# Optimization experiments

Measured on AMD Instinct MI355X. Metric: run time of the kernel, lower is better.

Reference implementation:

```python
import jax, jax.numpy as jnp
import numpy as np

# module hyperparams (init_kwargs)
OUTLINER_RATIO_1 = 0.01
OUTLINER_RATIO_2 = 0.01
SUB_OUTLINER_RATIO_2 = 0.2
SUB_OUTLINER_BIT_2 = 8
RANK = 16


def setup_inputs() -> dict:
    key = jax.random.key(0)
    k1, k2 = jax.random.split(key)
    B, H, S, D = 2, 16, 2048, 128
    # x1 is a softmax output (attention probabilities): rows sum to 1, values in [0,1]
    logits = jax.random.normal(k1, (B, H, S, S), dtype=jnp.float32)
    x1 = jax.nn.softmax(logits, axis=-1)
    x2 = jax.random.normal(k2, (B, H, S, D), dtype=jnp.float32)
    return {"x1": x1, "x2": x2}


def get_statistics_softmax(x, outliner_ratio):
    # kth-value threshold on first batch element (torch.kthvalue, 1-indexed)
    v = jnp.sort(x[0].reshape(-1))
    k = int(v.size * (1.0 - outliner_ratio))
    return v[k - 1]


def get_statistics_x2(x, outliner_ratio, sub_ratio, bit):
    x0 = x[0]  # [H, S, D]
    D = x0.shape[-1]
    a = jnp.abs(x0).reshape(-1)
    k = int(a.size * (1.0 - outliner_ratio))
    outliner = jnp.sort(a)[k - 1]
    # residual after removing outliers; rank columns by L2 norm
    resid = jnp.where(jnp.abs(x0) > outliner, 0.0, x0).reshape(-1, D)
    col_norm = jnp.linalg.norm(resid, axis=0)  # [D]
    n_cols = max(1, int(sub_ratio * D))
    _, cols = jax.lax.top_k(col_norm, n_cols)  # max-norm column list (static size)
    sub = resid[:, cols]
    qmax = float(2 ** (bit - 1) - 1)
    scale = jnp.max(jnp.abs(sub)) / qmax
    return outliner, cols, scale


def prune_softmax(x, outliner):
    return jnp.where(x > outliner, x, 0.0)


def fake_divide_outliner_suboutlinear_svd(x, outliner, cols, scale, rank, bit):
    # 1) split out outliers (kept exactly)
    x_out = jnp.where(jnp.abs(x) > outliner, x, 0.0)
    r = x - x_out
    # 2) rank-`rank` SVD approximation of the residual (batched over B,H)
    U, Sv, Vt = jnp.linalg.svd(r, full_matrices=False)
    x_lr = (U[..., :rank] * Sv[..., None, :rank]) @ Vt[..., :rank, :]
    r2 = r - x_lr
    # 3) fake-quantize the high-norm (sub-outlier) columns at `bit` bits; drop the rest
    qmax = float(2 ** (bit - 1) - 1)
    sub_q = jnp.clip(jnp.round(r2[..., cols] / scale), -qmax - 1.0, qmax) * scale
    r_q = jnp.zeros_like(r2).at[..., cols].set(sub_q)
    return x_out + x_lr + r_q


def reference(x1, x2):
    # iteration = 0 (< 10): compute statistics branch of EfficientMemoryGEMMWithSoftmaxFunc.forward
    result = x1 @ x2
    outliner_1 = get_statistics_softmax(x1, OUTLINER_RATIO_1)
    outliner_2, cols_2, scale_2 = get_statistics_x2(
        x2, OUTLINER_RATIO_2, SUB_OUTLINER_RATIO_2, SUB_OUTLINER_BIT_2)
    # The pruned/compressed tensors are computed (saved for backward in torch);
    # forward output matches Func.forward's returns.
    _x1p = prune_softmax(x1, outliner_1)
    _x2c = fake_divide_outliner_suboutlinear_svd(
        x2, outliner_2, cols_2, scale_2, RANK, SUB_OUTLINER_BIT_2)
    return (result, outliner_1, outliner_2, cols_2, scale_2)
```

## Files before the change

### kernel.cpp

```cpp
#include <hip/hip_runtime.h>

typedef __bf16 bf16x8 __attribute__((ext_vector_type(8)));
typedef unsigned short u16x8 __attribute__((ext_vector_type(8)));
typedef float f32x4 __attribute__((ext_vector_type(4)));

#define S_DIM 2048
#define D_DIM 128
#define N1 67108864LL
#define N2 4194304LL
#define RANK1 66437774u
#define RANK2 4152359u

#define OUT_O1 8388608
#define OUT_O2 8388609
#define OUT_COLS 8388610
#define OUT_SCALE 8388635

#define WS_H0 0
#define WS_H1 2048
#define WS_H2 4096
#define WS_H3 6144
#define WS_STATE 6656
#define WS_SUMSQ 6672
#define WS_CMAX 6800
#define WS_TICKET 6928
#define WS_TOTAL 8192

__device__ __forceinline__ unsigned long long pack4c(float x, float y, float z, float w) {
  union { unsigned long long u; __bf16 h[4]; } cv;
  cv.h[0] = (__bf16)x; cv.h[1] = (__bf16)y; cv.h[2] = (__bf16)z; cv.h[3] = (__bf16)w;
  return cv.u;
}

__global__ void init_ws(unsigned* __restrict__ ws) {
  int i = blockIdx.x * 256 + threadIdx.x;
  if (i < WS_TOTAL) ws[i] = (i == WS_STATE) ? RANK2 : 0u;
}

#define LDA 40

__global__ __launch_bounds__(256, 2) void gemm_kernel(
    const float* __restrict__ x1, const float* __restrict__ x2,
    float* __restrict__ out, unsigned* __restrict__ ws) {
  __shared__ __align__(16) unsigned short lA[128 * LDA];
  __shared__ __align__(16) unsigned short lB[128 * LDA];
  __shared__ unsigned lh[4][2048];
  __shared__ unsigned lh2[2048];
  __shared__ unsigned ps[256];
  __shared__ unsigned lastt;

  const int bid = blockIdx.x;
  const int bh = (bid & 7) + ((bid >> 7) << 3);
  const int mt = (bid >> 3) & 15;
  const int t = threadIdx.x;
  const int lane = t & 63;
  const int wave = t >> 6;
  const int wm = (wave >> 1) * 64;
  const int wn = (wave & 1) * 64;
  const int l15 = lane & 15;
  const int quad = lane >> 4;
  const bool do_hist = (bh < 16);

  unsigned* myh = lh[wave];
  if (do_hist) {
    for (int i = lane; i < 2048; i += 64) myh[i] = 0u;
    for (int i = t; i < 2048; i += 256) lh2[i] = 0u;
  }
  __syncthreads();

  const float* Ag = x1 + (long long)bh * S_DIM * S_DIM + (long long)mt * 128 * S_DIM;
  const float* Bg = x2 + (long long)bh * S_DIM * D_DIM;
  float* Cg = out + (long long)bh * S_DIM * D_DIM + (long long)mt * 128 * D_DIM;

  f32x4 acc[4][4];
#pragma unroll
  for (int i = 0; i < 4; ++i)
#pragma unroll
    for (int j = 0; j < 4; ++j) acc[i][j] = f32x4{0.f, 0.f, 0.f, 0.f};

  const int a_seg = t & 7;
  const int a_row = t >> 3;
  const int bcol = t & 127;
  const int b_kq = t >> 7;

  float4 a_c[4], b_c[4];
#pragma unroll
  for (int p = 0; p < 4; ++p)
    a_c[p] = *reinterpret_cast<const float4*>(Ag + (long long)(a_row + p * 32) * S_DIM + a_seg * 4);
#pragma unroll
  for (int g = 0; g < 4; ++g) {
    int k0 = b_kq * 16 + g * 4;
    long long base = (long long)k0 * D_DIM + bcol;
    b_c[g].x = Bg[base];
    b_c[g].y = Bg[base + D_DIM];
    b_c[g].z = Bg[base + 2 * D_DIM];
    b_c[g].w = Bg[base + 3 * D_DIM];
  }

  for (int kb = 0; kb < S_DIM; kb += 32) {
    float4 a_p[4], b_p[4];
    const bool pf = (kb + 32 < S_DIM);
    if (pf) {
#pragma unroll
      for (int p = 0; p < 4; ++p)
        a_p[p] = *reinterpret_cast<const float4*>(
            Ag + (long long)(a_row + p * 32) * S_DIM + (kb + 32) + a_seg * 4);
#pragma unroll
      for (int g = 0; g < 4; ++g) {
        int k0 = b_kq * 16 + g * 4;
        long long base = (long long)(kb + 32 + k0) * D_DIM + bcol;
        b_p[g].x = Bg[base];
        b_p[g].y = Bg[base + D_DIM];
        b_p[g].z = Bg[base + 2 * D_DIM];
        b_p[g].w = Bg[base + 3 * D_DIM];
      }
    }

#pragma unroll
    for (int p = 0; p < 4; ++p) {
      int row = a_row + p * 32;
      *reinterpret_cast<unsigned long long*>(&lA[row * LDA + a_seg * 4]) =
          pack4c(a_c[p].x, a_c[p].y, a_c[p].z, a_c[p].w);
    }
#pragma unroll
    for (int g = 0; g < 4; ++g) {
      int k0 = b_kq * 16 + g * 4;
      *reinterpret_cast<unsigned long long*>(&lB[bcol * LDA + k0]) =
          pack4c(b_c[g].x, b_c[g].y, b_c[g].z, b_c[g].w);
    }

    if (do_hist) {
#pragma unroll
      for (int p = 0; p < 4; ++p) {
        atomicAdd(&myh[__float_as_uint(a_c[p].x) >> 19], 1u);
        atomicAdd(&myh[__float_as_uint(a_c[p].y) >> 19], 1u);
        atomicAdd(&myh[__float_as_uint(a_c[p].z) >> 19], 1u);
        atomicAdd(&myh[__float_as_uint(a_c[p].w) >> 19], 1u);
      }
      if ((kb >> 7) == mt) {
#pragma unroll
        for (int g = 0; g < 4; ++g) {
          atomicAdd(&lh2[(__float_as_uint(b_c[g].x) & 0x7FFFFFFFu) >> 20], 1u);
          atomicAdd(&lh2[(__float_as_uint(b_c[g].y) & 0x7FFFFFFFu) >> 20], 1u);
          atomicAdd(&lh2[(__float_as_uint(b_c[g].z) & 0x7FFFFFFFu) >> 20], 1u);
          atomicAdd(&lh2[(__float_as_uint(b_c[g].w) & 0x7FFFFFFFu) >> 20], 1u);
        }
      }
    }
    __syncthreads();

    bf16x8 af[4], bfr[4];
#pragma unroll
    for (int i = 0; i < 4; ++i) {
      af[i] = __builtin_bit_cast(bf16x8,
          *reinterpret_cast<const u16x8*>(&lA[(wm + i * 16 + l15) * LDA + quad * 8]));
      bfr[i] = __builtin_bit_cast(bf16x8,
          *reinterpret_cast<const u16x8*>(&lB[(wn + i * 16 + l15) * LDA + quad * 8]));
    }
#pragma unroll
    for (int i = 0; i < 4; ++i)
#pragma unroll
      for (int j = 0; j < 4; ++j)
        acc[i][j] = __builtin_amdgcn_mfma_f32_16x16x32_bf16(af[i], bfr[j], acc[i][j], 0, 0, 0);
    __syncthreads();

    if (pf) {
#pragma unroll
      for (int p = 0; p < 4; ++p) a_c[p] = a_p[p];
#pragma unroll
      for (int g = 0; g < 4; ++g) b_c[g] = b_p[g];
    }
  }

#pragma unroll
  for (int i = 0; i < 4; ++i) {
#pragma unroll
    for (int j = 0; j < 4; ++j) {
      int row0 = wm + i * 16 + quad * 4;
      int col = wn + j * 16 + l15;
#pragma unroll
      for (int r = 0; r < 4; ++r)
        Cg[(long long)(row0 + r) * D_DIM + col] = acc[i][j][r];
    }
  }

  if (do_hist) {
    for (int i = t; i < 2048; i += 256) {
      unsigned s = lh[0][i] + lh[1][i] + lh[2][i] + lh[3][i];
      if (s) atomicAdd(&ws[WS_H0 + i], s);
      unsigned s2 = lh2[i];
      if (s2) atomicAdd(&ws[WS_H1 + i], s2);
    }
  }
  __threadfence();
  __syncthreads();
  if (t == 0) lastt = atomicAdd(&ws[WS_TICKET + 0], 1u);
  __syncthreads();
  if (lastt != 511u) return;

  {
    unsigned v[8];
    unsigned s = 0;
#pragma unroll
    for (int j = 0; j < 8; ++j) { v[j] = atomicAdd(&ws[WS_H0 + t * 8 + j], 0u); s += v[j]; }
    ps[t] = s;
    __syncthreads();
    for (int off = 1; off < 256; off <<= 1) {
      unsigned add = (t >= off) ? ps[t - off] : 0u;
      __syncthreads();
      ps[t] += add;
      __syncthreads();
    }
    unsigned incl = ps[t];
    unsigned before = incl - s;
    if (RANK1 >= before && RANK1 < incl) {
      unsigned rr = RANK1 - before;
      for (int j = 0; j < 8; ++j) {
        if (rr < v[j]) {
          unsigned b = (unsigned)(t * 8 + j);
          float lo = __uint_as_float(b << 19);
          float hi = __uint_as_float((b + 1u) << 19);
          out[OUT_O1] = lo + (hi - lo) * (((float)rr + 0.5f) / (float)v[j]);
          break;
        }
        rr -= v[j];
      }
    }
  }
  __syncthreads();

  {
    unsigned v[8];
    unsigned s = 0;
#pragma unroll
    for (int j = 0; j < 8; ++j) { v[j] = atomicAdd(&ws[WS_H1 + t * 8 + j], 0u); s += v[j]; }
    ps[t] = s;
    __syncthreads();
    for (int off = 1; off < 256; off <<= 1) {
      unsigned add = (t >= off) ? ps[t - off] : 0u;
      __syncthreads();
      ps[t] += add;
      __syncthreads();
    }
    unsigned incl = ps[t];
    unsigned before = incl - s;
    if (RANK2 >= before && RANK2 < incl) {
      unsigned rr = RANK2 - before;
      for (int j = 0; j < 8; ++j) {
        if (rr < v[j]) {
          ws[WS_STATE + 0] = rr;
          ws[WS_STATE + 1] = (unsigned)(t * 8 + j);
          break;
        }
        rr -= v[j];
      }
    }
  }
}

__global__ void x2_pass(const float* __restrict__ x2, unsigned* __restrict__ ws,
                        float* __restrict__ out, int phase) {
  __shared__ unsigned lh[2048];
  __shared__ unsigned ps[256];
  __shared__ unsigned lastt;
  unsigned* h = ws + ((phase == 2) ? WS_H2 : WS_H3);
  unsigned* state = ws + WS_STATE;
  const int nb = (phase == 3) ? 512 : 2048;
  const int t = threadIdx.x;
  for (int i = t; i < nb; i += 256) lh[i] = 0u;
  __syncthreads();
  const unsigned b1 = state[1];
  const unsigned pfx2 = (state[1] << 11) | state[2];
  long long i0 = (long long)(blockIdx.x * 256 + t) * 4;
  long long stride = (long long)gridDim.x * 1024;
  for (long long i = i0; i < N2; i += stride) {
    float4 v = *reinterpret_cast<const float4*>(x2 + i);
    float fv[4] = {v.x, v.y, v.z, v.w};
#pragma unroll
    for (int j = 0; j < 4; ++j) {
      unsigned key = __float_as_uint(fv[j]) & 0x7FFFFFFFu;
      if (phase == 2) {
        if ((key >> 20) == b1) atomicAdd(&lh[(key >> 9) & 0x7FFu], 1u);
      } else {
        if ((key >> 9) == pfx2) atomicAdd(&lh[key & 0x1FFu], 1u);
      }
    }
  }
  __syncthreads();
  for (int i = t; i < nb; i += 256)
    if (lh[i]) atomicAdd(&h[i], lh[i]);
  __threadfence();
  __syncthreads();
  if (t == 0) lastt = atomicAdd(&ws[WS_TICKET + ((phase == 2) ? 1 : 2)], 1u);
  __syncthreads();
  if (lastt != 255u) return;

  const int per = nb >> 8;
  const unsigned r = state[0];
  const unsigned sb1 = state[1];
  const unsigned sb2 = state[2];
  unsigned v[8];
  unsigned s = 0;
  for (int j = 0; j < per; ++j) { v[j] = atomicAdd(&h[t * per + j], 0u); s += v[j]; }
  ps[t] = s;
  __syncthreads();
  for (int off = 1; off < 256; off <<= 1) {
    unsigned add = (t >= off) ? ps[t - off] : 0u;
    __syncthreads();
    ps[t] += add;
    __syncthreads();
  }
  unsigned incl = ps[t];
  unsigned before = incl - s;
  if (r >= before && r < incl) {
    unsigned rr = r - before;
    for (int j = 0; j < per; ++j) {
      if (rr < v[j]) {
        unsigned b = (unsigned)(t * per + j);
        if (phase == 2) {
          state[0] = rr;
          state[2] = b;
        } else {
          unsigned bits = (sb1 << 20) | (sb2 << 9) | b;
          state[3] = bits;
          out[OUT_O2] = __uint_as_float(bits);
        }
        break;
      }
      rr -= v[j];
    }
  }
}

__global__ void colnorm_kernel(const float* __restrict__ x2, unsigned* __restrict__ ws,
                               float* __restrict__ out) {
  __shared__ float red[256];
  __shared__ unsigned redm[256];
  __shared__ float vv[128];
  __shared__ float rv[128];
  __shared__ int ri[128];
  __shared__ unsigned cmv[128];
  __shared__ unsigned lastt;
  unsigned* state = ws + WS_STATE;
  float* sumsq = (float*)(ws + WS_SUMSQ);
  unsigned* cmax = ws + WS_CMAX;
  const float thr = __uint_as_float(state[3]);
  const int t = threadIdx.x;
  const int c = t & 127;
  const int half = t >> 7;
  float local = 0.f;
  unsigned lmax = 0u;
  for (int i = 0; i < 64; ++i) {
    int row = blockIdx.x * 128 + i * 2 + half;
    float x = x2[(long long)row * 128 + c];
    float a = fabsf(x);
    if (a <= thr) {
      local += x * x;
      unsigned ab = __float_as_uint(a);
      if (ab > lmax) lmax = ab;
    }
  }
  red[t] = local;
  redm[t] = lmax;
  __syncthreads();
  if (half == 0) {
    atomicAdd(&sumsq[c], red[c] + red[c + 128]);
    unsigned m = redm[c] > redm[c + 128] ? redm[c] : redm[c + 128];
    if (m) atomicMax(&cmax[c], m);
  }
  __threadfence();
  __syncthreads();
  if (t == 0) lastt = atomicAdd(&ws[WS_TICKET + 3], 1u);
  __syncthreads();
  if (lastt != 255u) return;

  if (t < 128) {
    vv[t] = atomicAdd(&sumsq[t], 0.0f);
    cmv[t] = atomicMax(&cmax[t], 0u);
  }
  __syncthreads();
  unsigned smax = 0u;
  for (int s2 = 0; s2 < 25; ++s2) {
    if (t < 128) { rv[t] = vv[t]; ri[t] = t; }
    __syncthreads();
    for (int off = 64; off >= 1; off >>= 1) {
      if (t < off) {
        float a = rv[t], b = rv[t + off];
        int ia = ri[t], ib = ri[t + off];
        if (b > a || (b == a && ib < ia)) { rv[t] = b; ri[t] = ib; }
      }
      __syncthreads();
    }
    if (t == 0) {
      int cc = ri[0];
      out[OUT_COLS + s2] = (float)cc;
      vv[cc] = -1.0f;
      if (cmv[cc] > smax) smax = cmv[cc];
    }
    __syncthreads();
  }
  if (t == 0) out[OUT_SCALE] = __uint_as_float(smax) / 127.0f;
}

extern "C" void kernel_launch(void* const* d_in, const int* in_sizes, int n_in,
                              void* d_out, int out_size, void* d_ws, size_t ws_size,
                              hipStream_t stream) {
  (void)in_sizes; (void)n_in; (void)out_size; (void)ws_size;
  const float* x1 = (const float*)d_in[0];
  const float* x2 = (const float*)d_in[1];
  float* out = (float*)d_out;
  unsigned* ws = (unsigned*)d_ws;

  init_ws<<<32, 256, 0, stream>>>(ws);
  gemm_kernel<<<512, 256, 0, stream>>>(x1, x2, out, ws);
  x2_pass<<<256, 256, 0, stream>>>(x2, ws, out, 2);
  x2_pass<<<256, 256, 0, stream>>>(x2, ws, out, 3);
  colnorm_kernel<<<256, 256, 0, stream>>>(x2, ws, out);
}
```

Baseline: 927.0 us.

## Move x2 histogram and threshold finalization out of GEMM into separate pass

Removes the x2 magnitude histogram, the last-block ticket, and the softmax kth-value finalization from the GEMM kernel, and moves them into a new x2_pass1 kernel launched after the GEMM. The GEMM also drops its separate prefetch registers: it issues the next tile's global loads after the LDS stores and histogram atomics, so register pressure and shared memory use fall. The cost is one extra kernel launch and a second read of x2.

```diff
diff --git a/kernel.cpp b/kernel.cpp
--- a/kernel.cpp
+++ b/kernel.cpp
@@ -41,13 +41,10 @@
 
 __global__ __launch_bounds__(256, 2) void gemm_kernel(
     const float* __restrict__ x1, const float* __restrict__ x2,
-    float* __restrict__ out, unsigned* __restrict__ ws) {
+    float* __restrict__ out, unsigned* __restrict__ hist) {
   __shared__ __align__(16) unsigned short lA[128 * LDA];
   __shared__ __align__(16) unsigned short lB[128 * LDA];
   __shared__ unsigned lh[4][2048];
-  __shared__ unsigned lh2[2048];
-  __shared__ unsigned ps[256];
-  __shared__ unsigned lastt;
 
   const int bid = blockIdx.x;
   const int bh = (bid & 7) + ((bid >> 7) << 3);
@@ -64,9 +61,7 @@
   unsigned* myh = lh[wave];
   if (do_hist) {
     for (int i = lane; i < 2048; i += 64) myh[i] = 0u;
-    for (int i = t; i < 2048; i += 256) lh2[i] = 0u;
-  }
-  __syncthreads();
+  }
 
   const float* Ag = x1 + (long long)bh * S_DIM * S_DIM + (long long)mt * 128 * S_DIM;
   const float* Bg = x2 + (long long)bh * S_DIM * D_DIM;
@@ -80,71 +75,61 @@
 
   const int a_seg = t & 7;
   const int a_row = t >> 3;
-  const int bcol = t & 127;
+  const int b_n = t & 127;
   const int b_kq = t >> 7;
 
-  float4 a_c[4], b_c[4];
+  float4 a_r[4];
+  float4 b_r[4];
 #pragma unroll
   for (int p = 0; p < 4; ++p)
-    a_c[p] = *reinterpret_cast<const float4*>(Ag + (long long)(a_row + p * 32) * S_DIM + a_seg * 4);
+    a_r[p] = *reinterpret_cast<const float4*>(Ag + (long long)(a_row + p * 32) * S_DIM + a_seg * 4);
 #pragma unroll
   for (int g = 0; g < 4; ++g) {
     int k0 = b_kq * 16 + g * 4;
-    long long base = (long long)k0 * D_DIM + bcol;
-    b_c[g].x = Bg[base];
-    b_c[g].y = Bg[base + D_DIM];
-    b_c[g].z = Bg[base + 2 * D_DIM];
-    b_c[g].w = Bg[base + 3 * D_DIM];
+    long long base = (long long)k0 * D_DIM + b_n;
+    b_r[g].x = Bg[base];
+    b_r[g].y = Bg[base + D_DIM];
+    b_r[g].z = Bg[base + 2 * D_DIM];
+    b_r[g].w = Bg[base + 3 * D_DIM];
   }
 
   for (int kb = 0; kb < S_DIM; kb += 32) {
-    float4 a_p[4], b_p[4];
-    const bool pf = (kb + 32 < S_DIM);
-    if (pf) {
-#pragma unroll
-      for (int p = 0; p < 4; ++p)
-        a_p[p] = *reinterpret_cast<const float4*>(
-            Ag + (long long)(a_row + p * 32) * S_DIM + (kb + 32) + a_seg * 4);
-#pragma unroll
-      for (int g = 0; g < 4; ++g) {
-        int k0 = b_kq * 16 + g * 4;
-        long long base = (long long)(kb + 32 + k0) * D_DIM + bcol;
-        b_p[g].x = Bg[base];
-        b_p[g].y = Bg[base + D_DIM];
-        b_p[g].z = Bg[base + 2 * D_DIM];
-        b_p[g].w = Bg[base + 3 * D_DIM];
-      }
-    }
-
 #pragma unroll
     for (int p = 0; p < 4; ++p) {
       int row = a_row + p * 32;
       *reinterpret_cast<unsigned long long*>(&lA[row * LDA + a_seg * 4]) =
-          pack4c(a_c[p].x, a_c[p].y, a_c[p].z, a_c[p].w);
+          pack4c(a_r[p].x, a_r[p].y, a_r[p].z, a_r[p].w);
     }
 #pragma unroll
     for (int g = 0; g < 4; ++g) {
       int k0 = b_kq * 16 + g * 4;
-      *reinterpret_cast<unsigned long long*>(&lB[bcol * LDA + k0]) =
-          pack4c(b_c[g].x, b_c[g].y, b_c[g].z, b_c[g].w);
+      *reinterpret_cast<unsigned long long*>(&lB[b_n * LDA + k0]) =
+          pack4c(b_r[g].x, b_r[g].y, b_r[g].z, b_r[g].w);
     }
 
     if (do_hist) {
 #pragma unroll
       for (int p = 0; p < 4; ++p) {
-        atomicAdd(&myh[__float_as_uint(a_c[p].x) >> 19], 1u);
-        atomicAdd(&myh[__float_as_uint(a_c[p].y) >> 19], 1u);
-        atomicAdd(&myh[__float_as_uint(a_c[p].z) >> 19], 1u);
-        atomicAdd(&myh[__float_as_uint(a_c[p].w) >> 19], 1u);
-      }
-      if ((kb >> 7) == mt) {
-#pragma unroll
-        for (int g = 0; g < 4; ++g) {
-          atomicAdd(&lh2[(__float_as_uint(b_c[g].x) & 0x7FFFFFFFu) >> 20], 1u);
-          atomicAdd(&lh2[(__float_as_uint(b_c[g].y) & 0x7FFFFFFFu) >> 20], 1u);
-          atomicAdd(&lh2[(__float_as_uint(b_c[g].z) & 0x7FFFFFFFu) >> 20], 1u);
-          atomicAdd(&lh2[(__float_as_uint(b_c[g].w) & 0x7FFFFFFFu) >> 20], 1u);
-        }
+        atomicAdd(&myh[__float_as_uint(a_r[p].x) >> 19], 1u);
+        atomicAdd(&myh[__float_as_uint(a_r[p].y) >> 19], 1u);
+        atomicAdd(&myh[__float_as_uint(a_r[p].z) >> 19], 1u);
+        atomicAdd(&myh[__float_as_uint(a_r[p].w) >> 19], 1u);
+      }
+    }
+
+    if (kb + 32 < S_DIM) {
+#pragma unroll
+      for (int p = 0; p < 4; ++p)
+        a_r[p] = *reinterpret_cast<const float4*>(
+            Ag + (long long)(a_row + p * 32) * S_DIM + (kb + 32) + a_seg * 4);
+#pragma unroll
+      for (int g = 0; g < 4; ++g) {
+        int k0 = b_kq * 16 + g * 4;
+        long long base = (long long)(kb + 32 + k0) * D_DIM + b_n;
+        b_r[g].x = Bg[base];
+        b_r[g].y = Bg[base + D_DIM];
+        b_r[g].z = Bg[base + 2 * D_DIM];
+        b_r[g].w = Bg[base + 3 * D_DIM];
       }
     }
     __syncthreads();
@@ -163,13 +148,6 @@
       for (int j = 0; j < 4; ++j)
         acc[i][j] = __builtin_amdgcn_mfma_f32_16x16x32_bf16(af[i], bfr[j], acc[i][j], 0, 0, 0);
     __syncthreads();
-
-    if (pf) {
-#pragma unroll
-      for (int p = 0; p < 4; ++p) a_c[p] = a_p[p];
-#pragma unroll
-      for (int g = 0; g < 4; ++g) b_c[g] = b_p[g];
-    }
   }
 
 #pragma unroll
@@ -187,22 +165,42 @@
   if (do_hist) {
     for (int i = t; i < 2048; i += 256) {
       unsigned s = lh[0][i] + lh[1][i] + lh[2][i] + lh[3][i];
-      if (s) atomicAdd(&ws[WS_H0 + i], s);
-      unsigned s2 = lh2[i];
-      if (s2) atomicAdd(&ws[WS_H1 + i], s2);
-    }
-  }
+      if (s) atomicAdd(&hist[i], s);
+    }
+  }
+}
+
+__global__ void x2_pass1(const float* __restrict__ x2, unsigned* __restrict__ ws,
+                         float* __restrict__ out) {
+  __shared__ unsigned lh[2048];
+  __shared__ unsigned ps[256];
+  __shared__ unsigned lastt;
+  const int t = threadIdx.x;
+  for (int i = t; i < 2048; i += 256) lh[i] = 0u;
+  __syncthreads();
+  long long i0 = (long long)(blockIdx.x * 256 + t) * 4;
+  long long stride = (long long)gridDim.x * 1024;
+  for (long long i = i0; i < N2; i += stride) {
+    float4 v = *reinterpret_cast<const float4*>(x2 + i);
+    atomicAdd(&lh[(__float_as_uint(v.x) & 0x7FFFFFFFu) >> 20], 1u);
+    atomicAdd(&lh[(__float_as_uint(v.y) & 0x7FFFFFFFu) >> 20], 1u);
+    atomicAdd(&lh[(__float_as_uint(v.z) & 0x7FFFFFFFu) >> 20], 1u);
+    atomicAdd(&lh[(__float_as_uint(v.w) & 0x7FFFFFFFu) >> 20], 1u);
+  }
+  __syncthreads();
+  for (int i = t; i < 2048; i += 256)
+    if (lh[i]) atomicAdd(&ws[WS_H1 + i], lh[i]);
   __threadfence();
   __syncthreads();
   if (t == 0) lastt = atomicAdd(&ws[WS_TICKET + 0], 1u);
   __syncthreads();
-  if (lastt != 511u) return;
+  if (lastt != 255u) return;
 
   {
     unsigned v[8];
     unsigned s = 0;
 #pragma unroll
-    for (int j = 0; j < 8; ++j) { v[j] = atomicAdd(&ws[WS_H0 + t * 8 + j], 0u); s += v[j]; }
+    for (int j = 0; j < 8; ++j) { v[j] = ws[WS_H0 + t * 8 + j]; s += v[j]; }
     ps[t] = s;
     __syncthreads();
     for (int off = 1; off < 256; off <<= 1) {
@@ -412,7 +410,8 @@
   unsigned* ws = (unsigned*)d_ws;
 
   init_ws<<<32, 256, 0, stream>>>(ws);
-  gemm_kernel<<<512, 256, 0, stream>>>(x1, x2, out, ws);
+  gemm_kernel<<<512, 256, 0, stream>>>(x1, x2, out, ws + WS_H0);
+  x2_pass1<<<256, 256, 0, stream>>>(x2, ws, out);
   x2_pass<<<256, 256, 0, stream>>>(x2, ws, out, 2);
   x2_pass<<<256, 256, 0, stream>>>(x2, ws, out, 3);
   colnorm_kernel<<<256, 256, 0, stream>>>(x2, ws, out);
```

After: 874.5 us. -5.7%, faster.
